# Kernel tuning notes

Measured on AMD Instinct MI355X. Metric: run time of the kernel, lower is better.

## Reference

```python
import jax, jax.numpy as jnp
import numpy as np

N = 100000
E = 1600000
IN_DIM = 128
OUT_DIM = 128
NEG_SLOPE = 0.01  # F.leaky_relu default


def setup_inputs() -> dict:
    key = jax.random.key(0)
    k1, k2, k3, k4, k5, k6 = jax.random.split(key, 6)
    feat = jax.random.normal(k1, (N, IN_DIM), dtype=jnp.float32)
    biclique_mask = jax.random.uniform(k2, (IN_DIM,), dtype=jnp.float32)
    W = jax.random.normal(k3, (OUT_DIM, IN_DIM), dtype=jnp.float32) * 0.05
    attn = jax.random.normal(k4, (OUT_DIM,), dtype=jnp.float32) * 0.1
    src = jax.random.randint(k5, (E,), 0, N, dtype=jnp.int32)
    dst = jax.random.randint(k6, (E,), 0, N, dtype=jnp.int32)
    return {"feat": feat, "biclique_mask": biclique_mask, "W": W,
            "attn": attn, "src": src, "dst": dst}


def reference(feat, biclique_mask, W, attn, src, dst):
    # h = Linear(feat * mask), no bias
    h = (feat * biclique_mask[None, :]) @ W.T            # [N, out_dim]
    # edge score depends only on src node -> compute per-node then gather
    s = jax.nn.leaky_relu(h @ attn, negative_slope=NEG_SLOPE)  # [N]
    score = s[src]                                        # [E]
    # edge softmax grouped by destination node
    seg_max = jax.ops.segment_max(score, dst, num_segments=N)  # [N]
    seg_max = jnp.where(jnp.isfinite(seg_max), seg_max, 0.0)   # empty segs
    ex = jnp.exp(score - seg_max[dst])                     # [E]
    denom = jax.ops.segment_sum(ex, dst, num_segments=N)   # [N]
    a = ex / denom[dst]                                    # [E]
    # weighted aggregation: sum_{e: dst(e)=v} h[src(e)] * a[e]
    m = h[src] * a[:, None]                                # [E, out_dim]
    h_new = jax.ops.segment_sum(m, dst, num_segments=N)    # [N, out_dim]
    return jax.nn.relu(h_new)
```

## Files before the change

### kernel.cpp

```cpp
#include <hip/hip_runtime.h>
#include <math.h>

#define NN 100000
#define EE 1600000
#define DIM 128

#define BK 256
#define NBK2 392
#define NCH 256
#define EPB 6250
#define SCN (NBK2 * NCH)
#define NSB 98

#define GEMM_BLKS 1563

#define SRC_MASK 0x1FFFFu

typedef _Float16 half8 __attribute__((ext_vector_type(8)));
typedef signed char char8 __attribute__((ext_vector_type(8)));
typedef float f32x4 __attribute__((ext_vector_type(4)));

__global__ __launch_bounds__(256) void k_wt(const float* __restrict__ W,
                                            const float* __restrict__ mask,
                                            _Float16* __restrict__ Bt) {
    int o = blockIdx.x * 256 + threadIdx.x;
    if (o < DIM * DIM) Bt[o] = (_Float16)(W[o] * mask[o & 127]);
}

__global__ __launch_bounds__(256) void k_front(const float* __restrict__ feat,
                                               const _Float16* __restrict__ Bt,
                                               const float* __restrict__ attn,
                                               signed char* __restrict__ hq,
                                               float* __restrict__ scf,
                                               _Float16* __restrict__ sv16,
                                               const int* __restrict__ dst,
                                               int* __restrict__ gHist) {
    __shared__ int hist[NBK2];
    const int bx = blockIdx.x;
    const int t  = threadIdx.x;

    if (bx >= GEMM_BLKS) {
        const int b = bx - GEMM_BLKS;
        for (int i = t; i < NBK2; i += 256) hist[i] = 0;
        __syncthreads();
        const int e0 = b * EPB;
        int e1 = e0 + EPB; if (e1 > EE) e1 = EE;
        for (int e = e0 + t; e < e1; e += 256)
            atomicAdd(&hist[dst[e] >> 8], 1);
        __syncthreads();
        for (int i = t; i < NBK2; i += 256)
            gHist[i * NCH + b] = hist[i];
        return;
    }

    const int lane = t & 63;
    const int wv   = t >> 6;
    const int l15  = lane & 15;
    const int quad = lane >> 4;
    const int row0 = bx * 64 + wv * 16;

    f32x4 acc[8];
#pragma unroll
    for (int nt = 0; nt < 8; ++nt) acc[nt] = (f32x4){0.f, 0.f, 0.f, 0.f};

    const int arow = row0 + l15;
    const bool okA = arow < NN;
    const float* ap = feat + (size_t)(okA ? arow : 0) * DIM + quad * 8;

#pragma unroll
    for (int kc = 0; kc < 4; ++kc) {
        half8 a;
        float4 f0 = ((const float4*)(ap + kc * 32))[0];
        float4 f1 = ((const float4*)(ap + kc * 32))[1];
        if (!okA) { f0 = make_float4(0, 0, 0, 0); f1 = make_float4(0, 0, 0, 0); }
        a[0] = (_Float16)f0.x; a[1] = (_Float16)f0.y;
        a[2] = (_Float16)f0.z; a[3] = (_Float16)f0.w;
        a[4] = (_Float16)f1.x; a[5] = (_Float16)f1.y;
        a[6] = (_Float16)f1.z; a[7] = (_Float16)f1.w;
#pragma unroll
        for (int nt = 0; nt < 8; ++nt) {
            half8 b = *(const half8*)(Bt + (size_t)(nt * 16 + l15) * DIM + kc * 32 + quad * 8);
            acc[nt] = __builtin_amdgcn_mfma_f32_16x16x32_f16(a, b, acc[nt], 0, 0, 0);
        }
    }

    float avv[8];
#pragma unroll
    for (int nt = 0; nt < 8; ++nt) avv[nt] = attn[nt * 16 + l15];

#pragma unroll
    for (int r = 0; r < 4; ++r) {
        int row = row0 + quad * 4 + r;
        float p = 0.f, m = 0.f;
#pragma unroll
        for (int nt = 0; nt < 8; ++nt) {
            p += acc[nt][r] * avv[nt];
            m = fmaxf(m, fabsf(acc[nt][r]));
        }
        p += __shfl_xor(p, 1, 64);
        p += __shfl_xor(p, 2, 64);
        p += __shfl_xor(p, 4, 64);
        p += __shfl_xor(p, 8, 64);
        m = fmaxf(m, __shfl_xor(m, 1, 64));
        m = fmaxf(m, __shfl_xor(m, 2, 64));
        m = fmaxf(m, __shfl_xor(m, 4, 64));
        m = fmaxf(m, __shfl_xor(m, 8, 64));
        if (l15 == 0 && row < NN) {
            float lr = (p > 0.f) ? p : 0.01f * p;
            sv16[row] = (_Float16)__expf(lr);
            scf[row]  = m * (1.f / 127.f);
        }
        const float inv_s = (m > 0.f) ? (127.f / m) : 0.f;
        if (row < NN) {
#pragma unroll
            for (int nt = 0; nt < 8; ++nt) {
                float qv = rintf(acc[nt][r] * inv_s);
                qv = fminf(fmaxf(qv, -127.f), 127.f);
                hq[(size_t)row * DIM + nt * 16 + l15] = (signed char)(int)qv;
            }
        }
    }
}

__global__ __launch_bounds__(256) void k_scan_a(const int* __restrict__ deg,
                                                int* __restrict__ excl,
                                                int* __restrict__ bsum) {
    __shared__ int wsum[4];
    __shared__ int woff[4];
    const int t = threadIdx.x, b = blockIdx.x;
    const int base = b * 1024 + t * 4;
    int v0 = deg[base + 0];
    int v1 = deg[base + 1];
    int v2 = deg[base + 2];
    int v3 = deg[base + 3];
    int tsum = v0 + v1 + v2 + v3;

    const int lane = t & 63, w = t >> 6;
    int incl = tsum;
#pragma unroll
    for (int d = 1; d < 64; d <<= 1) {
        int n = __shfl_up(incl, d, 64);
        if (lane >= d) incl += n;
    }
    if (lane == 63) wsum[w] = incl;
    __syncthreads();
    if (t == 0) {
        int run = 0;
#pragma unroll
        for (int i = 0; i < 4; ++i) { woff[i] = run; run += wsum[i]; }
        bsum[b] = run;
    }
    __syncthreads();
    int texcl = incl - tsum + woff[w];
    excl[base + 0] = texcl;
    excl[base + 1] = texcl + v0;
    excl[base + 2] = texcl + v0 + v1;
    excl[base + 3] = texcl + v0 + v1 + v2;
}

#define INLINE_BOFF_SCAN(bsum, sboff, swtop, t)                          \
    {                                                                    \
        const int lane_ = (t) & 63;                                      \
        int v_ = 0, incl_ = 0;                                           \
        if ((t) < 128) {                                                 \
            v_ = ((t) < NSB) ? (bsum)[(t)] : 0;                          \
            incl_ = v_;                                                  \
            _Pragma("unroll")                                            \
            for (int d_ = 1; d_ < 64; d_ <<= 1) {                        \
                int n_ = __shfl_up(incl_, d_, 64);                       \
                if (lane_ >= d_) incl_ += n_;                            \
            }                                                            \
            if ((t) == 63) (swtop) = incl_;                              \
        }                                                                \
        __syncthreads();                                                 \
        if ((t) < NSB) {                                                 \
            int add_ = ((t) >= 64) ? (swtop) : 0;                        \
            (sboff)[(t)] = incl_ - v_ + add_;                            \
        }                                                                \
        __syncthreads();                                                 \
    }

__global__ __launch_bounds__(1024) void k_bscatter(const int* __restrict__ src,
                                                   const int* __restrict__ dst,
                                                   const int* __restrict__ gOff,
                                                   const int* __restrict__ bsum,
                                                   unsigned* __restrict__ binned) {
    __shared__ int cur[NBK2];
    __shared__ int sboff[NSB];
    __shared__ int swtop;
    const int t = threadIdx.x, b = blockIdx.x;

    INLINE_BOFF_SCAN(bsum, sboff, swtop, t)

    for (int i = t; i < NBK2; i += 1024) {
        int idx = i * NCH + b;
        cur[i] = gOff[idx] + sboff[idx >> 10];
    }
    __syncthreads();
    const int e0 = b * EPB;
    int e1 = e0 + EPB; if (e1 > EE) e1 = EE;
    for (int e = e0 + t; e < e1; e += 1024) {
        int d  = dst[e];
        int si = src[e];
        int bk   = d >> 8;
        int dloc = d & (BK - 1);
        int pos = atomicAdd(&cur[bk], 1);
        binned[pos] = (unsigned)si | ((unsigned)dloc << 17);
    }
}

__global__ __launch_bounds__(1024) void k_group(const int* __restrict__ gOff,
                                                const int* __restrict__ bsum,
                                                const unsigned* __restrict__ binned,
                                                const _Float16* __restrict__ sv16,
                                                const float* __restrict__ scf,
                                                unsigned* __restrict__ pack,
                                                int* __restrict__ offs,
                                                float* __restrict__ lsum) {
    __shared__ int ldeg[BK];
    __shared__ float lsumSh[BK];
    __shared__ int wpart[4];
    __shared__ int sboff[NSB];
    __shared__ int swtop;
    const int bk = blockIdx.x;
    const int t  = threadIdx.x;

    INLINE_BOFF_SCAN(bsum, sboff, swtop, t)

    const int i0 = bk * NCH;
    const int base = gOff[i0] + sboff[i0 >> 10];
    int endp;
    if (bk == NBK2 - 1) endp = EE;
    else {
        int i1 = (bk + 1) * NCH;
        endp = gOff[i1] + sboff[i1 >> 10];
    }

    if (t < BK) { ldeg[t] = 0; lsumSh[t] = 0.f; }
    __syncthreads();
    for (int j = base + t; j < endp; j += 1024)
        atomicAdd(&ldeg[(binned[j] >> 17) & (BK - 1)], 1);
    __syncthreads();

    int v = 0, incl = 0;
    const int lane = t & 63;
    if (t < BK) {
        v = ldeg[t];
        incl = v;
#pragma unroll
        for (int d = 1; d < 64; d <<= 1) {
            int n = __shfl_up(incl, d, 64);
            if (lane >= d) incl += n;
        }
        if (lane == 63) wpart[t >> 6] = incl;
    }
    __syncthreads();
    if (t == 0) {
        int run = 0;
#pragma unroll
        for (int i = 0; i < 4; ++i) { int tmp = wpart[i]; wpart[i] = run; run += tmp; }
    }
    __syncthreads();
    if (t < BK) {
        int excl = incl - v + wpart[t >> 6];
        int c = base + excl;
        int n = bk * BK + t;
        if (n < NN) offs[n] = c;
        ldeg[t] = c;
    }
    if (bk == NBK2 - 1 && t == 0) offs[NN] = EE;
    __syncthreads();

    for (int j = base + t; j < endp; j += 1024) {
        unsigned e = binned[j];
        int dloc = (e >> 17) & (BK - 1);
        int si   = e & SRC_MASK;
        float w  = (float)sv16[si];
        float sc = scf[si];
        unsigned short wb =
            __builtin_bit_cast(unsigned short, (_Float16)(w * sc));
        atomicAdd(&lsumSh[dloc], w);
        int pos = atomicAdd(&ldeg[dloc], 1);
        pack[pos] = (unsigned)si | ((unsigned)wb << 17);
    }
    __syncthreads();
    if (t < BK) {
        int n = bk * BK + t;
        if (n < NN) lsum[n] = lsumSh[t];
    }
}

__global__ __launch_bounds__(256) void k_agg(const signed char* __restrict__ hq,
                                             const int* __restrict__ offs,
                                             const unsigned* __restrict__ pack,
                                             const float* __restrict__ lsum,
                                             float* __restrict__ out) {
    const int lane = threadIdx.x & 63;
    const int g    = lane >> 4;
    const int li   = lane & 15;
    const int wid  = __builtin_amdgcn_readfirstlane(blockIdx.x * 4 + (threadIdx.x >> 6));
    if (wid >= NN) return;
    const int beg = __builtin_amdgcn_readfirstlane(offs[wid]);
    const int end = __builtin_amdgcn_readfirstlane(offs[wid + 1]);
    const int deg = end - beg;

    float acc[8];
#pragma unroll
    for (int k = 0; k < 8; ++k) acc[k] = 0.f;

    for (int base = 0; base < deg; base += 64) {
        const int nrem = deg - base;
        const int idx  = base + lane;
        const int cl   = (idx < deg) ? idx : (deg - 1);
        const unsigned eraw = pack[beg + cl];
        const unsigned enc = (idx < deg) ? eraw : (eraw & SRC_MASK);
        const int cmax = (nrem < 64) ? nrem : 64;
        for (int c0 = 0; c0 < cmax; c0 += 16) {
#pragma unroll
            for (int s = 0; s < 4; ++s) {
                const int ei = c0 + s * 4 + g;
                const unsigned eb =
                    (unsigned)__shfl((int)enc, ei, 64);
                const int   si = eb & SRC_MASK;
                const float wg = (float)__builtin_bit_cast(
                    _Float16, (unsigned short)(eb >> 17));
                char8 q = *(const char8*)(hq + ((size_t)(unsigned)si << 7) + li * 8);
#pragma unroll
                for (int k = 0; k < 8; ++k)
                    acc[k] = fmaf((float)q[k], wg, acc[k]);
            }
        }
    }

#pragma unroll
    for (int k = 0; k < 8; ++k) {
        acc[k] += __shfl_xor(acc[k], 16, 64);
        acc[k] += __shfl_xor(acc[k], 32, 64);
    }

    const float l   = lsum[wid];
    const float inv = (l > 0.f) ? (1.0f / l) : 0.f;

    if (g == 0) {
        float4 o0, o1;
        o0.x = fmaxf(acc[0] * inv, 0.f);
        o0.y = fmaxf(acc[1] * inv, 0.f);
        o0.z = fmaxf(acc[2] * inv, 0.f);
        o0.w = fmaxf(acc[3] * inv, 0.f);
        o1.x = fmaxf(acc[4] * inv, 0.f);
        o1.y = fmaxf(acc[5] * inv, 0.f);
        o1.z = fmaxf(acc[6] * inv, 0.f);
        o1.w = fmaxf(acc[7] * inv, 0.f);
        float4* op = (float4*)(out + (size_t)wid * DIM + li * 8);
        op[0] = o0;
        op[1] = o1;
    }
}

extern "C" void kernel_launch(void* const* d_in, const int* in_sizes, int n_in,
                              void* d_out, int out_size, void* d_ws, size_t ws_size,
                              hipStream_t stream) {
    const float* feat = (const float*)d_in[0];
    const float* mask = (const float*)d_in[1];
    const float* W    = (const float*)d_in[2];
    const float* attn = (const float*)d_in[3];
    const int*   src  = (const int*)d_in[4];
    const int*   dst  = (const int*)d_in[5];
    float* out = (float*)d_out;

    char* ws = (char*)d_ws;
    size_t off = 0;
    auto alloc = [&](size_t bytes) -> void* {
        void* p = ws + off;
        off = (off + bytes + 511) & ~(size_t)511;
        return p;
    };
    signed char* hq  = (signed char*)alloc((size_t)NN * DIM);
    float*   scf  = (float*)alloc((size_t)NN * 4);
    float*   lsum = (float*)alloc((size_t)NN * 4);
    _Float16* sv16 = (_Float16*)alloc((size_t)NN * 2);
    _Float16* Bt   = (_Float16*)alloc((size_t)DIM * DIM * 2);
    int*     gOff  = (int*)alloc((size_t)SCN * 4);
    int*     offs  = (int*)alloc((size_t)(NN + 1) * 4);
    int*     bsum  = (int*)alloc((size_t)NSB * 4);
    unsigned* binned = (unsigned*)alloc((size_t)EE * 4);
    unsigned* pack   = (unsigned*)alloc((size_t)EE * 4);

    k_wt<<<(DIM * DIM + 255) / 256, 256, 0, stream>>>(W, mask, Bt);
    k_front<<<GEMM_BLKS + NCH, 256, 0, stream>>>(feat, Bt, attn, hq, scf,
                                                 sv16, dst, gOff);
    k_scan_a<<<NSB, 256, 0, stream>>>(gOff, gOff, bsum);
    k_bscatter<<<NCH, 1024, 0, stream>>>(src, dst, gOff, bsum, binned);
    k_group<<<NBK2, 1024, 0, stream>>>(gOff, bsum, binned, sv16, scf,
                                       pack, offs, lsum);
    k_agg<<<(NN + 3) / 4, 256, 0, stream>>>(hq, offs, pack, lsum, out);
}
```

Measured before the change: 222.2 us.

## Stage GEMM operands in LDS and coalesce int8 output stores in k_front

The front GEMM kernel now uses 512-thread blocks that each cover 128 rows. Each block loads its feature tile (converted to fp16) and the full weight matrix into padded LDS with coalesced float4/int4 loads, and the MFMA loop reads its operands from LDS. Quantized int8 results are first written to an LDS slice per wave, then written to global memory as 32-byte vector stores per lane instead of scattered byte stores. This targets uncoalesced global loads and stores, at the cost of 68KB of LDS per block, which limits how many blocks can be resident per CU.

Result: faster. 206.1 us (-7.2%).

```diff
diff --git a/kernel.cpp b/kernel.cpp
--- a/kernel.cpp
+++ b/kernel.cpp
@@ -12,11 +12,17 @@
 #define SCN (NBK2 * NCH)
 #define NSB 98
 
-#define GEMM_BLKS 1563
+#define GEMM_BLKS 782
+#define FBLK 512
+
+#define LDS_ROW 272
+#define LDS_B_OFF 34816
+#define LDS_TOT 69632
 
 #define SRC_MASK 0x1FFFFu
 
 typedef _Float16 half8 __attribute__((ext_vector_type(8)));
+typedef _Float16 half4v __attribute__((ext_vector_type(4)));
 typedef signed char char8 __attribute__((ext_vector_type(8)));
 typedef float f32x4 __attribute__((ext_vector_type(4)));
 
@@ -27,59 +33,78 @@
     if (o < DIM * DIM) Bt[o] = (_Float16)(W[o] * mask[o & 127]);
 }
 
-__global__ __launch_bounds__(256) void k_front(const float* __restrict__ feat,
-                                               const _Float16* __restrict__ Bt,
-                                               const float* __restrict__ attn,
-                                               signed char* __restrict__ hq,
-                                               float* __restrict__ scf,
-                                               _Float16* __restrict__ sv16,
-                                               const int* __restrict__ dst,
-                                               int* __restrict__ gHist) {
-    __shared__ int hist[NBK2];
+__global__ __launch_bounds__(512, 4) void k_front(const float* __restrict__ feat,
+                                                  const _Float16* __restrict__ Bt,
+                                                  const float* __restrict__ attn,
+                                                  signed char* __restrict__ hq,
+                                                  float* __restrict__ scf,
+                                                  _Float16* __restrict__ sv16,
+                                                  const int* __restrict__ dst,
+                                                  int* __restrict__ gHist) {
+    __shared__ char smem[LDS_TOT];
     const int bx = blockIdx.x;
     const int t  = threadIdx.x;
 
     if (bx >= GEMM_BLKS) {
+        int* hist = (int*)smem;
         const int b = bx - GEMM_BLKS;
-        for (int i = t; i < NBK2; i += 256) hist[i] = 0;
+        for (int i = t; i < NBK2; i += FBLK) hist[i] = 0;
         __syncthreads();
         const int e0 = b * EPB;
         int e1 = e0 + EPB; if (e1 > EE) e1 = EE;
-        for (int e = e0 + t; e < e1; e += 256)
+        for (int e = e0 + t; e < e1; e += FBLK)
             atomicAdd(&hist[dst[e] >> 8], 1);
         __syncthreads();
-        for (int i = t; i < NBK2; i += 256)
+        for (int i = t; i < NBK2; i += FBLK)
             gHist[i * NCH + b] = hist[i];
         return;
     }
+
+    const int rowBase = bx * 128;
+
+#pragma unroll
+    for (int i = 0; i < 8; ++i) {
+        int idx  = i * FBLK + t;
+        int r    = idx >> 5;
+        int c4   = idx & 31;
+        int rowg = rowBase + r;
+        float4 f = (rowg < NN)
+                       ? ((const float4*)(feat + (size_t)rowg * DIM))[c4]
+                       : make_float4(0.f, 0.f, 0.f, 0.f);
+        half4v h;
+        h[0] = (_Float16)f.x; h[1] = (_Float16)f.y;
+        h[2] = (_Float16)f.z; h[3] = (_Float16)f.w;
+        *(half4v*)(smem + r * LDS_ROW + c4 * 8) = h;
+    }
+#pragma unroll
+    for (int i = 0; i < 4; ++i) {
+        int idx = i * FBLK + t;
+        int r   = idx >> 4;
+        int c8  = idx & 15;
+        int4 v = ((const int4*)(Bt + (size_t)r * DIM))[c8];
+        *(int4*)(smem + LDS_B_OFF + r * LDS_ROW + c8 * 16) = v;
+    }
+    __syncthreads();
 
     const int lane = t & 63;
     const int wv   = t >> 6;
     const int l15  = lane & 15;
     const int quad = lane >> 4;
-    const int row0 = bx * 64 + wv * 16;
+    const int row0 = rowBase + wv * 16;
 
     f32x4 acc[8];
 #pragma unroll
     for (int nt = 0; nt < 8; ++nt) acc[nt] = (f32x4){0.f, 0.f, 0.f, 0.f};
 
-    const int arow = row0 + l15;
-    const bool okA = arow < NN;
-    const float* ap = feat + (size_t)(okA ? arow : 0) * DIM + quad * 8;
+    const char* Abase = smem + (wv * 16 + l15) * LDS_ROW + quad * 16;
+    const char* Bbase = smem + LDS_B_OFF + l15 * LDS_ROW + quad * 16;
 
 #pragma unroll
     for (int kc = 0; kc < 4; ++kc) {
-        half8 a;
-        float4 f0 = ((const float4*)(ap + kc * 32))[0];
-        float4 f1 = ((const float4*)(ap + kc * 32))[1];
-        if (!okA) { f0 = make_float4(0, 0, 0, 0); f1 = make_float4(0, 0, 0, 0); }
-        a[0] = (_Float16)f0.x; a[1] = (_Float16)f0.y;
-        a[2] = (_Float16)f0.z; a[3] = (_Float16)f0.w;
-        a[4] = (_Float16)f1.x; a[5] = (_Float16)f1.y;
-        a[6] = (_Float16)f1.z; a[7] = (_Float16)f1.w;
+        half8 a = *(const half8*)(Abase + kc * 64);
 #pragma unroll
         for (int nt = 0; nt < 8; ++nt) {
-            half8 b = *(const half8*)(Bt + (size_t)(nt * 16 + l15) * DIM + kc * 32 + quad * 8);
+            half8 b = *(const half8*)(Bbase + nt * 16 * LDS_ROW + kc * 64);
             acc[nt] = __builtin_amdgcn_mfma_f32_16x16x32_f16(a, b, acc[nt], 0, 0, 0);
         }
     }
@@ -88,6 +113,7 @@
 #pragma unroll
     for (int nt = 0; nt < 8; ++nt) avv[nt] = attn[nt * 16 + l15];
 
+    char* qslice = smem + wv * (16 * LDS_ROW);
 #pragma unroll
     for (int r = 0; r < 4; ++r) {
         int row = row0 + quad * 4 + r;
@@ -111,13 +137,21 @@
             scf[row]  = m * (1.f / 127.f);
         }
         const float inv_s = (m > 0.f) ? (127.f / m) : 0.f;
-        if (row < NN) {
-#pragma unroll
-            for (int nt = 0; nt < 8; ++nt) {
-                float qv = rintf(acc[nt][r] * inv_s);
-                qv = fminf(fmaxf(qv, -127.f), 127.f);
-                hq[(size_t)row * DIM + nt * 16 + l15] = (signed char)(int)qv;
-            }
+#pragma unroll
+        for (int nt = 0; nt < 8; ++nt) {
+            float qv = rintf(acc[nt][r] * inv_s);
+            qv = fminf(fmaxf(qv, -127.f), 127.f);
+            qslice[(quad * 4 + r) * 128 + nt * 16 + l15] = (signed char)(int)qv;
+        }
+    }
+    {
+        const int rowg = row0 + (lane >> 2);
+        if (rowg < NN) {
+            int4 v0 = *(const int4*)(qslice + lane * 32);
+            int4 v1 = *(const int4*)(qslice + lane * 32 + 16);
+            int4* dp = (int4*)(hq + (size_t)rowg * DIM + (lane & 3) * 32);
+            dp[0] = v0;
+            dp[1] = v1;
         }
     }
 }
@@ -387,8 +421,8 @@
     unsigned* pack   = (unsigned*)alloc((size_t)EE * 4);
 
     k_wt<<<(DIM * DIM + 255) / 256, 256, 0, stream>>>(W, mask, Bt);
-    k_front<<<GEMM_BLKS + NCH, 256, 0, stream>>>(feat, Bt, attn, hq, scf,
-                                                 sv16, dst, gOff);
+    k_front<<<GEMM_BLKS + NCH, FBLK, 0, stream>>>(feat, Bt, attn, hq, scf,
+                                                  sv16, dst, gOff);
     k_scan_a<<<NSB, 256, 0, stream>>>(gOff, gOff, bsum);
     k_bscatter<<<NCH, 1024, 0, stream>>>(src, dst, gOff, bsum, binned);
     k_group<<<NBK2, 1024, 0, stream>>>(gOff, bsum, binned, sv16, scf,
```
